# Performance work log

Measured on AMD Instinct MI355X. Metric: run time of the kernel, lower is better.

Reference implementation:

```python
import jax, jax.numpy as jnp
import numpy as np

IN_C = 64
OUT_C = 128
K = 3          # kernel_size = (3, 3)
STRIDE = 1
PAD = 2        # total padding, split as pad_l = PAD//2, pad_r = PAD - pad_l
BRANCH = 3
ACCL = IN_C * K * K  # 576


def setup_inputs() -> dict:
    key = jax.random.key(0)
    k1, k2, k3, k4 = jax.random.split(key, 4)
    x = jax.random.normal(k1, (16, IN_C, 64, 64), dtype=jnp.float32)
    # kaiming_uniform-like scale for fan_in = branch^2
    bound1 = 1.0 / np.sqrt(BRANCH * BRANCH)
    bound2 = 1.0 / np.sqrt(BRANCH)
    w1 = jax.random.uniform(k2, (OUT_C, BRANCH * BRANCH), jnp.float32, -bound1, bound1)
    w2 = jax.random.uniform(k3, (OUT_C, BRANCH), jnp.float32, -bound2, bound2)
    conn = jax.random.randint(k4, (OUT_C * BRANCH * BRANCH,), 0, ACCL, dtype=jnp.int32)
    return {"x": x, "w1": w1, "w2": w2, "conn": conn}


def reference(x, w1, w2, conn):
    pad_l = PAD // 2
    pad_r = PAD - pad_l
    # replicate padding on H, W
    x_pad = jnp.pad(x, ((0, 0), (0, 0), (pad_l, pad_r), (pad_l, pad_r)), mode='edge')
    B, C, Hp, Wp = x_pad.shape
    Hout = (Hp - K) // STRIDE + 1
    Wout = (Wp - K) // STRIDE + 1
    # im2col patches: last axis ordered (kh, kw) with kw fastest -> [B,C,Hout,Wout,K*K]
    pats = jnp.stack(
        [x_pad[:, :, i:i + (Hout - 1) * STRIDE + 1:STRIDE,
                     j:j + (Wout - 1) * STRIDE + 1:STRIDE]
         for i in range(K) for j in range(K)],
        axis=-1)
    # [B,Hout,Wout,C*K*K], flattened as (C, kh, kw) matching torch reshape
    pats = pats.transpose(0, 2, 3, 1, 4).reshape(B, Hout, Wout, C * K * K)
    # random gather over kernel-position/channel axis -> [B,Hout,Wout,O,branch^2]
    g = pats[..., conn].reshape(B, Hout, Wout, OUT_C, BRANCH * BRANCH)
    g = g.transpose(0, 3, 1, 2, 4)  # [B,O,Hout,Wout,branch^2]
    d = g - w1[:, None, None, :]    # broadcast over B,H,W
    ma = jnp.max(d.reshape(d.shape[:-1] + (BRANCH, BRANCH)), axis=-1)  # [B,O,H,W,branch]
    mi = jnp.min(ma - w2[:, None, None, :], axis=-1)                    # [B,O,H,W]
    return mi
```

## Files before the change

kernel.cpp:

```cpp
#include <hip/hip_runtime.h>


#define IN_C  64
#define OUT_C 128
#define HH    64
#define WW    64
#define TH    4
#define TW    32
#define LR    (TH + 2)
#define LCV   (TW + 2)
#define LC    40
#define CHS   245
#define NTHR  512

__global__ __launch_bounds__(NTHR, 4)
void minimax_conv_kernel(const float* __restrict__ x,
                         const float* __restrict__ w1,
                         const float* __restrict__ w2,
                         const int*   __restrict__ conn,
                         float*       __restrict__ out) {
    __shared__ float xs[IN_C * CHS];

    const int tid  = threadIdx.x;
    const int wt   = blockIdx.x;
    const int ht   = blockIdx.y;
    const int b    = blockIdx.z;
    const int h0   = ht * TH;
    const int w0   = wt * TW;

    const int lane = tid & 63;
    const int wid  = __builtin_amdgcn_readfirstlane(tid >> 6);
    const int chg  = wid & 1;
    const int r    = wid >> 1;
    const int o    = chg * 64 + lane;

    int   dlt[9]; float w1v[9]; float w2v[3];
    #pragma unroll
    for (int t = 0; t < 9; ++t) {
        const int idx = conn[o * 9 + t];
        const int c   = idx / 9;
        const int k   = idx - 9 * c;
        const int kh  = k / 3;
        const int kw  = k - 3 * kh;
        dlt[t] = c * CHS + kh * LC + kw;
        w1v[t] = w1[o * 9 + t];
    }
    #pragma unroll
    for (int p = 0; p < 3; ++p) w2v[p] = w2[o * 3 + p];

    const float* xb = x + (size_t)b * IN_C * HH * WW;
    for (int i = tid; i < IN_C * LR * LCV; i += NTHR) {
        int c  = i / (LR * LCV);
        int rm = i - c * (LR * LCV);
        int rr = rm / LCV;
        int cc = rm - rr * LCV;
        int gh = h0 + rr - 1; gh = gh < 0 ? 0 : (gh > HH - 1 ? HH - 1 : gh);
        int gw = w0 + cc - 1; gw = gw < 0 ? 0 : (gw > WW - 1 ? WW - 1 : gw);
        xs[c * CHS + rr * LC + cc] = xb[(c * HH + gh) * WW + gw];
    }
    __syncthreads();

    const int base = r * LC;
    float vout[32];

    #pragma unroll
    for (int c0 = 0; c0 < 16; ++c0) {
        float a[9][2];
        #pragma unroll
        for (int t = 0; t < 9; ++t) {
            const int ad = base + c0 + dlt[t];
            a[t][0] = xs[ad];
            a[t][1] = xs[ad + 16];
        }
        #pragma unroll
        for (int px = 0; px < 2; ++px) {
            float mi = 0.0f;
            #pragma unroll
            for (int p = 0; p < 3; ++p) {
                float ma = a[p * 3 + 0][px] - w1v[p * 3 + 0];
                ma = fmaxf(ma, a[p * 3 + 1][px] - w1v[p * 3 + 1]);
                ma = fmaxf(ma, a[p * 3 + 2][px] - w1v[p * 3 + 2]);
                const float t2 = ma - w2v[p];
                mi = (p == 0) ? t2 : fminf(mi, t2);
            }
            vout[c0 + px * 16] = mi;
        }
    }

    float* op = out + (((size_t)b * OUT_C + o) * HH + (h0 + r)) * WW + w0;
    #pragma unroll
    for (int q = 0; q < 8; ++q) {
        *reinterpret_cast<float4*>(op + q * 4) =
            make_float4(vout[4 * q], vout[4 * q + 1], vout[4 * q + 2], vout[4 * q + 3]);
    }
}

extern "C" void kernel_launch(void* const* d_in, const int* in_sizes, int n_in,
                              void* d_out, int out_size, void* d_ws, size_t ws_size,
                              hipStream_t stream) {
    const float* x    = (const float*)d_in[0];
    const float* w1   = (const float*)d_in[1];
    const float* w2   = (const float*)d_in[2];
    const int*   conn = (const int*)d_in[3];
    float*       out  = (float*)d_out;

    dim3 grid(WW / TW, HH / TH, 16);
    minimax_conv_kernel<<<grid, NTHR, 0, stream>>>(x, w1, w2, conn, out);
}
```

Measured before the change: 97.28 us.

## Remap threads to pixels with wave-uniform output channels via precomputed table

Adds a small pre-kernel that packs per-output-channel gather offsets and w1/w2 weights into a workspace table. The main kernel now assigns each wave 16 output channels and lays its lanes out over pixels (4 rows x 16 columns), so each table entry is wave-uniform and can be read with scalar/broadcast loads, and the LDS reads for neighbouring pixels fall on consecutive addresses instead of being scattered by per-lane random offsets. Stores become coalesced scalar writes per channel rather than per-thread float4 rows. The costs are an extra kernel launch, and LDS padding now changes CHS to 240, which may alter bank-conflict behaviour for the staging writes.

```diff
diff --git a/kernel.cpp b/kernel.cpp
--- a/kernel.cpp
+++ b/kernel.cpp
@@ -10,31 +10,16 @@
 #define LR    (TH + 2)
 #define LCV   (TW + 2)
 #define LC    40
-#define CHS   245
+#define CHS   (LR * LC)
 #define NTHR  512
+#define TABS  24
 
-__global__ __launch_bounds__(NTHR, 4)
-void minimax_conv_kernel(const float* __restrict__ x,
-                         const float* __restrict__ w1,
-                         const float* __restrict__ w2,
-                         const int*   __restrict__ conn,
-                         float*       __restrict__ out) {
-    __shared__ float xs[IN_C * CHS];
-
-    const int tid  = threadIdx.x;
-    const int wt   = blockIdx.x;
-    const int ht   = blockIdx.y;
-    const int b    = blockIdx.z;
-    const int h0   = ht * TH;
-    const int w0   = wt * TW;
-
-    const int lane = tid & 63;
-    const int wid  = __builtin_amdgcn_readfirstlane(tid >> 6);
-    const int chg  = wid & 1;
-    const int r    = wid >> 1;
-    const int o    = chg * 64 + lane;
-
-    int   dlt[9]; float w1v[9]; float w2v[3];
+__global__ __launch_bounds__(128)
+void build_tab(const int* __restrict__ conn, const float* __restrict__ w1,
+               const float* __restrict__ w2, int* __restrict__ tab) {
+    const int o = threadIdx.x;
+    int*   tp = tab + o * TABS;
+    float* fp = (float*)tp;
     #pragma unroll
     for (int t = 0; t < 9; ++t) {
         const int idx = conn[o * 9 + t];
@@ -42,11 +27,25 @@
         const int k   = idx - 9 * c;
         const int kh  = k / 3;
         const int kw  = k - 3 * kh;
-        dlt[t] = c * CHS + kh * LC + kw;
-        w1v[t] = w1[o * 9 + t];
+        tp[t]     = c * CHS + kh * LC + kw;
+        fp[9 + t] = w1[o * 9 + t];
     }
     #pragma unroll
-    for (int p = 0; p < 3; ++p) w2v[p] = w2[o * 3 + p];
+    for (int p = 0; p < 3; ++p) fp[18 + p] = w2[o * 3 + p];
+    tp[21] = 0; tp[22] = 0; tp[23] = 0;
+}
+
+__global__ __launch_bounds__(NTHR, 4)
+void mm_main(const float* __restrict__ x, const int* __restrict__ tab,
+             float* __restrict__ out) {
+    __shared__ float xs[IN_C * CHS];
+
+    const int tid = threadIdx.x;
+    const int wt  = blockIdx.x;
+    const int ht  = blockIdx.y;
+    const int b   = blockIdx.z;
+    const int h0  = ht * TH;
+    const int w0  = wt * TW;
 
     const float* xb = x + (size_t)b * IN_C * HH * WW;
     for (int i = tid; i < IN_C * LR * LCV; i += NTHR) {
@@ -60,38 +59,96 @@
     }
     __syncthreads();
 
-    const int base = r * LC;
-    float vout[32];
+    const int lane  = tid & 63;
+    const int wid_v = tid >> 6;
+    const int wid   = __builtin_amdgcn_readfirstlane(wid_v);
+    const int r     = lane >> 4;
+    const int cc    = lane & 15;
+    const int base  = r * LC + cc;
 
-    #pragma unroll
-    for (int c0 = 0; c0 < 16; ++c0) {
-        float a[9][2];
+    const int4* tw = (const int4*)(tab + wid_v * (16 * TABS));
+
+    float* op = out + ((((size_t)b * OUT_C + wid * 16) * HH) + (h0 + r)) * WW + (w0 + cc);
+
+    for (int oo = 0; oo < 16; oo += 2) {
+        const int4 I0 = tw[oo * 6 + 0];
+        const int4 I1 = tw[oo * 6 + 1];
+        const int4 I2 = tw[oo * 6 + 2];
+        const int4 I3 = tw[oo * 6 + 3];
+        const int4 I4 = tw[oo * 6 + 4];
+        const int4 I5 = tw[oo * 6 + 5];
+        const int4 J0 = tw[oo * 6 + 6];
+        const int4 J1 = tw[oo * 6 + 7];
+        const int4 J2 = tw[oo * 6 + 8];
+        const int4 J3 = tw[oo * 6 + 9];
+        const int4 J4 = tw[oo * 6 + 10];
+        const int4 J5 = tw[oo * 6 + 11];
+
+        float a0[9], a1[9], b0[9], b1[9];
+        {
+            const int d[9] = { I0.x, I0.y, I0.z, I0.w, I1.x, I1.y, I1.z, I1.w, I2.x };
+            #pragma unroll
+            for (int t = 0; t < 9; ++t) {
+                const int ad = base + d[t];
+                a0[t] = xs[ad];
+                a1[t] = xs[ad + 16];
+            }
+        }
+        {
+            const int d[9] = { J0.x, J0.y, J0.z, J0.w, J1.x, J1.y, J1.z, J1.w, J2.x };
+            #pragma unroll
+            for (int t = 0; t < 9; ++t) {
+                const int ad = base + d[t];
+                b0[t] = xs[ad];
+                b1[t] = xs[ad + 16];
+            }
+        }
+
+        const float w1a[9] = { __int_as_float(I2.y), __int_as_float(I2.z), __int_as_float(I2.w),
+                               __int_as_float(I3.x), __int_as_float(I3.y), __int_as_float(I3.z),
+                               __int_as_float(I3.w), __int_as_float(I4.x), __int_as_float(I4.y) };
+        const float w2a[3] = { __int_as_float(I4.z), __int_as_float(I4.w), __int_as_float(I5.x) };
+        const float w1b[9] = { __int_as_float(J2.y), __int_as_float(J2.z), __int_as_float(J2.w),
+                               __int_as_float(J3.x), __int_as_float(J3.y), __int_as_float(J3.z),
+                               __int_as_float(J3.w), __int_as_float(J4.x), __int_as_float(J4.y) };
+        const float w2b[3] = { __int_as_float(J4.z), __int_as_float(J4.w), __int_as_float(J5.x) };
+
         #pragma unroll
-        for (int t = 0; t < 9; ++t) {
-            const int ad = base + c0 + dlt[t];
-            a[t][0] = xs[ad];
-            a[t][1] = xs[ad + 16];
+        for (int px = 0; px < 2; ++px) {
+            const float* a = px ? a1 : a0;
+            float ma, mi;
+            ma = a[0] - w1a[0];
+            ma = fmaxf(ma, a[1] - w1a[1]);
+            ma = fmaxf(ma, a[2] - w1a[2]);
+            mi = ma - w2a[0];
+            ma = a[3] - w1a[3];
+            ma = fmaxf(ma, a[4] - w1a[4]);
+            ma = fmaxf(ma, a[5] - w1a[5]);
+            mi = fminf(mi, ma - w2a[1]);
+            ma = a[6] - w1a[6];
+            ma = fmaxf(ma, a[7] - w1a[7]);
+            ma = fmaxf(ma, a[8] - w1a[8]);
+            mi = fminf(mi, ma - w2a[2]);
+            op[(size_t)oo * (HH * WW) + px * 16] = mi;
         }
         #pragma unroll
         for (int px = 0; px < 2; ++px) {
-            float mi = 0.0f;
-            #pragma unroll
-            for (int p = 0; p < 3; ++p) {
-                float ma = a[p * 3 + 0][px] - w1v[p * 3 + 0];
-                ma = fmaxf(ma, a[p * 3 + 1][px] - w1v[p * 3 + 1]);
-                ma = fmaxf(ma, a[p * 3 + 2][px] - w1v[p * 3 + 2]);
-                const float t2 = ma - w2v[p];
-                mi = (p == 0) ? t2 : fminf(mi, t2);
-            }
-            vout[c0 + px * 16] = mi;
+            const float* a = px ? b1 : b0;
+            float ma, mi;
+            ma = a[0] - w1b[0];
+            ma = fmaxf(ma, a[1] - w1b[1]);
+            ma = fmaxf(ma, a[2] - w1b[2]);
+            mi = ma - w2b[0];
+            ma = a[3] - w1b[3];
+            ma = fmaxf(ma, a[4] - w1b[4]);
+            ma = fmaxf(ma, a[5] - w1b[5]);
+            mi = fminf(mi, ma - w2b[1]);
+            ma = a[6] - w1b[6];
+            ma = fmaxf(ma, a[7] - w1b[7]);
+            ma = fmaxf(ma, a[8] - w1b[8]);
+            mi = fminf(mi, ma - w2b[2]);
+            op[(size_t)(oo + 1) * (HH * WW) + px * 16] = mi;
         }
-    }
-
-    float* op = out + (((size_t)b * OUT_C + o) * HH + (h0 + r)) * WW + w0;
-    #pragma unroll
-    for (int q = 0; q < 8; ++q) {
-        *reinterpret_cast<float4*>(op + q * 4) =
-            make_float4(vout[4 * q], vout[4 * q + 1], vout[4 * q + 2], vout[4 * q + 3]);
     }
 }
 
@@ -103,7 +160,10 @@
     const float* w2   = (const float*)d_in[2];
     const int*   conn = (const int*)d_in[3];
     float*       out  = (float*)d_out;
+    int*         tab  = (int*)d_ws;
+
+    build_tab<<<1, 128, 0, stream>>>(conn, w1, w2, tab);
 
     dim3 grid(WW / TW, HH / TH, 16);
-    minimax_conv_kernel<<<grid, NTHR, 0, stream>>>(x, w1, w2, conn, out);
+    mm_main<<<grid, NTHR, 0, stream>>>(x, tab, out);
 }
```

After: 98.10 us. About the same (+0.8%).
